# Kernel optimization log

Hardware: AMD Instinct MI355X
Metric: run time of the kernel (lower is better)

Reference implementation:

```python
import jax, jax.numpy as jnp
import numpy as np

B, H, S, D = 16, 12, 1024, 64  # batch, heads, seq, head_dim (dim=768, num_head=12)


def setup_inputs() -> dict:
    key = jax.random.key(0)
    ks = jax.random.split(key, 9)
    sc = 1.0 / np.sqrt(D)
    return {
        "x": jax.random.normal(ks[0], (B, H, S, D), dtype=jnp.float32),
        "Wq": jax.random.normal(ks[1], (D, D), dtype=jnp.float32) * sc,
        "bq": jax.random.normal(ks[2], (D,), dtype=jnp.float32) * 0.02,
        "Wk": jax.random.normal(ks[3], (D, D), dtype=jnp.float32) * sc,
        "bk": jax.random.normal(ks[4], (D,), dtype=jnp.float32) * 0.02,
        "Wv": jax.random.normal(ks[5], (D, D), dtype=jnp.float32) * sc,
        "bv": jax.random.normal(ks[6], (D,), dtype=jnp.float32) * 0.02,
        "Wo": jax.random.normal(ks[7], (D, D), dtype=jnp.float32) * sc,
        "bo": jax.random.normal(ks[8], (D,), dtype=jnp.float32) * 0.02,
    }


def reference(x, Wq, bq, Wk, bk, Wv, bv, Wo, bo):
    # torch Linear: y = x @ W^T + b, applied to last dim (head_dim)
    q = jnp.einsum("bhsd,ed->bhse", x, Wq) + bq
    k = jnp.einsum("bhsd,ed->bhse", x, Wk) + bk
    v = jnp.einsum("bhsd,ed->bhse", x, Wv) + bv
    scores = jnp.einsum("bhqd,bhkd->bhqk", q, k) / jnp.sqrt(jnp.float32(q.shape[-1]))
    attn = jax.nn.softmax(scores, axis=-1)
    out = jnp.einsum("bhqk,bhkd->bhqd", attn, v)
    out = jnp.einsum("bhsd,ed->bhse", out, Wo) + bo
    return out
```

## Files before the change

### kernel.cpp

```cpp
#include <hip/hip_runtime.h>
#include <math.h>


typedef __bf16 bf16x8 __attribute__((ext_vector_type(8)));
typedef float  f32x4  __attribute__((ext_vector_type(4)));

#define MFMA(a, b, c) __builtin_amdgcn_mfma_f32_16x16x32_bf16((a), (b), (c), 0, 0, 0)

static constexpr int S = 1024;
static constexpr int PAD = 72;
static constexpr size_t NE = 196608ull * 64ull;
static constexpr float QSCALE = 0.125f * 1.4426950408889634f;

__device__ inline unsigned long long pack4bf(float a, float b, float c, float d) {
    union { __bf16 h[4]; unsigned long long u; } pk;
    pk.h[0] = (__bf16)a; pk.h[1] = (__bf16)b; pk.h[2] = (__bf16)c; pk.h[3] = (__bf16)d;
    return pk.u;
}

__global__ void wo_conv(const float* __restrict__ Wo, __bf16* __restrict__ wob) {
    int i = (blockIdx.x * 256 + threadIdx.x) * 4;
    float4 v = *(const float4*)(Wo + i);
    *(unsigned long long*)(wob + i) = pack4bf(v.x, v.y, v.z, v.w);
}

__global__ __launch_bounds__(256) void proj_qkv(
    const float* __restrict__ x,
    const float* __restrict__ Wq, const float* __restrict__ bq,
    const float* __restrict__ Wk, const float* __restrict__ bk,
    const float* __restrict__ Wv, const float* __restrict__ bv,
    __bf16* __restrict__ gq, __bf16* __restrict__ gk, __bf16* __restrict__ gvt)
{
    __shared__ __align__(16) __bf16 lx[128][PAD];
    __shared__ __align__(16) __bf16 lw[3][64][PAD];
    __shared__ __align__(16) __bf16 lbuf[128][PAD];
    __shared__ float lb[3][64];

    const int tid = threadIdx.x;
    const int row_base = blockIdx.x * 128;

    #pragma unroll
    for (int i = tid * 4; i < 8192; i += 1024) {
        float4 v = *(const float4*)(x + (size_t)row_base * 64 + i);
        int r = i >> 6, c = i & 63;
        *(unsigned long long*)&lx[r][c] = pack4bf(v.x, v.y, v.z, v.w);
    }
    const float* Ws[3] = {Wq, Wk, Wv};
    #pragma unroll
    for (int mtx = 0; mtx < 3; mtx++) {
        #pragma unroll
        for (int i = tid * 4; i < 4096; i += 1024) {
            float4 v = *(const float4*)(Ws[mtx] + i);
            int r = i >> 6, c = i & 63;
            *(unsigned long long*)&lw[mtx][r][c] = pack4bf(v.x, v.y, v.z, v.w);
        }
    }
    if (tid < 64) { lb[0][tid] = bq[tid]; lb[1][tid] = bk[tid]; lb[2][tid] = bv[tid]; }
    __syncthreads();

    const int w = tid >> 6, lane = tid & 63, m = lane & 15, quad = lane >> 4;
    const int bh = row_base >> 10;
    const int s_base = row_base & 1023;

    bf16x8 xf[2][2];
    #pragma unroll
    for (int g = 0; g < 2; g++) {
        xf[g][0] = *(const bf16x8*)&lx[w * 32 + g * 16 + m][quad * 8];
        xf[g][1] = *(const bf16x8*)&lx[w * 32 + g * 16 + m][32 + quad * 8];
    }

    #pragma unroll
    for (int mtx = 0; mtx < 2; mtx++) {
        #pragma unroll
        for (int et = 0; et < 4; et++) {
            bf16x8 wf0 = *(const bf16x8*)&lw[mtx][et * 16 + m][quad * 8];
            bf16x8 wf1 = *(const bf16x8*)&lw[mtx][et * 16 + m][32 + quad * 8];
            float4 bias = *(const float4*)&lb[mtx][et * 16 + quad * 4];
            #pragma unroll
            for (int g = 0; g < 2; g++) {
                f32x4 acc = {0.f, 0.f, 0.f, 0.f};
                acc = MFMA(wf0, xf[g][0], acc);
                acc = MFMA(wf1, xf[g][1], acc);
                unsigned long long u;
                if (mtx == 0)
                    u = pack4bf((acc[0] + bias.x) * QSCALE, (acc[1] + bias.y) * QSCALE,
                                (acc[2] + bias.z) * QSCALE, (acc[3] + bias.w) * QSCALE);
                else
                    u = pack4bf(acc[0] + bias.x, acc[1] + bias.y,
                                acc[2] + bias.z, acc[3] + bias.w);
                *(unsigned long long*)&lbuf[w * 32 + g * 16 + m][et * 16 + quad * 4] = u;
            }
        }
        __syncthreads();
        __bf16* dst = (mtx == 0 ? gq : gk);
        #pragma unroll
        for (int it = 0; it < 4; it++) {
            int idx = it * 256 + tid;
            int row = idx >> 3, col = (idx & 7) * 8;
            *(uint4*)(dst + ((size_t)row_base + row) * 64 + col) = *(uint4*)&lbuf[row][col];
        }
        __syncthreads();
    }

    __bf16 (*lvt)[136] = (__bf16(*)[136])&lbuf[0][0];
    #pragma unroll
    for (int et = 0; et < 4; et++) {
        bf16x8 wf0 = *(const bf16x8*)&lw[2][et * 16 + m][quad * 8];
        bf16x8 wf1 = *(const bf16x8*)&lw[2][et * 16 + m][32 + quad * 8];
        const float bias = lb[2][et * 16 + m];
        #pragma unroll
        for (int g = 0; g < 2; g++) {
            f32x4 acc = {0.f, 0.f, 0.f, 0.f};
            acc = MFMA(xf[g][0], wf0, acc);
            acc = MFMA(xf[g][1], wf1, acc);
            *(unsigned long long*)&lvt[et * 16 + m][w * 32 + g * 16 + quad * 4] =
                pack4bf(acc[0] + bias, acc[1] + bias, acc[2] + bias, acc[3] + bias);
        }
    }
    __syncthreads();
    #pragma unroll
    for (int it = 0; it < 4; it++) {
        int idx = it * 256 + tid;
        int row = idx >> 4, col = (idx & 15) * 8;
        *(uint4*)(gvt + ((size_t)bh * 64 + row) * 1024 + s_base + col) = *(uint4*)&lvt[row][col];
    }
}

__global__ __launch_bounds__(256) void attn(
    const __bf16* __restrict__ gq, const __bf16* __restrict__ gk,
    const __bf16* __restrict__ gvt, const __bf16* __restrict__ wob,
    const float* __restrict__ bo, float* __restrict__ out)
{
    __shared__ __align__(16) __bf16 lk[64][PAD];
    __shared__ __align__(16) __bf16 lv[64][PAD];
    __shared__ __align__(16) __bf16 lp[4][32][PAD];

    const int tid = threadIdx.x;
    const int w = tid >> 6, lane = tid & 63, m = lane & 15, quad = lane >> 4;
    const int bh = blockIdx.x;
    const int q0 = blockIdx.y * 256 + w * 64;

    bf16x8 qf[4][2];
    #pragma unroll
    for (int g = 0; g < 4; g++) {
        const __bf16* qrow = gq + ((size_t)bh * S + q0 + g * 16 + m) * 64;
        qf[g][0] = *(const bf16x8*)(qrow + quad * 8);
        qf[g][1] = *(const bf16x8*)(qrow + 32 + quad * 8);
    }

    f32x4 o[4][4];
    float lsum[4] = {0.f, 0.f, 0.f, 0.f};
    #pragma unroll
    for (int g = 0; g < 4; g++)
        #pragma unroll
        for (int n = 0; n < 4; n++) o[g][n] = {0.f, 0.f, 0.f, 0.f};

    const int sr = tid >> 3;
    const int sc = (tid & 7) * 8;
    const __bf16* kbase = gk + (size_t)bh * S * 64;
    const __bf16* vbase = gvt + (size_t)bh * 64 * 1024;

    uint4 kreg0 = *(const uint4*)(kbase + (size_t)sr * 64 + sc);
    uint4 kreg1 = *(const uint4*)(kbase + (size_t)(sr + 32) * 64 + sc);
    uint4 vreg0 = *(const uint4*)(vbase + (size_t)sr * 1024 + sc);
    uint4 vreg1 = *(const uint4*)(vbase + (size_t)(sr + 32) * 1024 + sc);

    for (int kb = 0; kb < 16; kb++) {
        __syncthreads();
        *(uint4*)&lk[sr][sc]      = kreg0;
        *(uint4*)&lk[sr + 32][sc] = kreg1;
        *(uint4*)&lv[sr][sc]      = vreg0;
        *(uint4*)&lv[sr + 32][sc] = vreg1;
        if (kb < 15) {
            const int nb = (kb + 1) * 64;
            kreg0 = *(const uint4*)(kbase + (size_t)(nb + sr) * 64 + sc);
            kreg1 = *(const uint4*)(kbase + (size_t)(nb + sr + 32) * 64 + sc);
            vreg0 = *(const uint4*)(vbase + (size_t)sr * 1024 + nb + sc);
            vreg1 = *(const uint4*)(vbase + (size_t)(sr + 32) * 1024 + nb + sc);
        }
        __syncthreads();

        #pragma unroll
        for (int gp = 0; gp < 2; gp++) {
            #pragma unroll
            for (int t = 0; t < 4; t++) {
                bf16x8 ka0 = *(const bf16x8*)&lk[t * 16 + m][quad * 8];
                bf16x8 ka1 = *(const bf16x8*)&lk[t * 16 + m][32 + quad * 8];
                #pragma unroll
                for (int gl = 0; gl < 2; gl++) {
                    const int g = gp * 2 + gl;
                    f32x4 acc = {0.f, 0.f, 0.f, 0.f};
                    acc = MFMA(ka0, qf[g][0], acc);
                    acc = MFMA(ka1, qf[g][1], acc);
                    float e0 = __builtin_amdgcn_exp2f(acc[0]);
                    float e1 = __builtin_amdgcn_exp2f(acc[1]);
                    float e2 = __builtin_amdgcn_exp2f(acc[2]);
                    float e3 = __builtin_amdgcn_exp2f(acc[3]);
                    lsum[g] += (e0 + e1) + (e2 + e3);
                    *(unsigned long long*)&lp[w][gl * 16 + m][t * 16 + quad * 4] =
                        pack4bf(e0, e1, e2, e3);
                }
            }
            bf16x8 pb[2][2];
            #pragma unroll
            for (int gl = 0; gl < 2; gl++) {
                pb[gl][0] = *(const bf16x8*)&lp[w][gl * 16 + m][quad * 8];
                pb[gl][1] = *(const bf16x8*)&lp[w][gl * 16 + m][32 + quad * 8];
            }
            #pragma unroll
            for (int n = 0; n < 4; n++) {
                bf16x8 va0 = *(const bf16x8*)&lv[n * 16 + m][quad * 8];
                bf16x8 va1 = *(const bf16x8*)&lv[n * 16 + m][32 + quad * 8];
                #pragma unroll
                for (int gl = 0; gl < 2; gl++) {
                    const int g = gp * 2 + gl;
                    o[g][n] = MFMA(va0, pb[gl][0], o[g][n]);
                    o[g][n] = MFMA(va1, pb[gl][1], o[g][n]);
                }
            }
        }
    }

    bf16x8 wf[4][2];
    #pragma unroll
    for (int et = 0; et < 4; et++) {
        wf[et][0] = *(const bf16x8*)(wob + (size_t)(et * 16 + m) * 64 + quad * 8);
        wf[et][1] = *(const bf16x8*)(wob + (size_t)(et * 16 + m) * 64 + 32 + quad * 8);
    }
    float biasr[4];
    #pragma unroll
    for (int et = 0; et < 4; et++) biasr[et] = bo[et * 16 + m];

    #pragma unroll
    for (int g = 0; g < 4; g++) {
        lsum[g] += __shfl_xor(lsum[g], 16);
        lsum[g] += __shfl_xor(lsum[g], 32);
    }

    #pragma unroll
    for (int gp = 0; gp < 2; gp++) {
        #pragma unroll
        for (int gl = 0; gl < 2; gl++) {
            const int g = gp * 2 + gl;
            const float inv = 1.f / lsum[g];
            #pragma unroll
            for (int n = 0; n < 4; n++) {
                *(unsigned long long*)&lp[w][gl * 16 + m][n * 16 + quad * 4] =
                    pack4bf(o[g][n][0] * inv, o[g][n][1] * inv,
                            o[g][n][2] * inv, o[g][n][3] * inv);
            }
        }
        #pragma unroll
        for (int gl = 0; gl < 2; gl++) {
            const int g = gp * 2 + gl;
            bf16x8 af0 = *(const bf16x8*)&lp[w][gl * 16 + m][quad * 8];
            bf16x8 af1 = *(const bf16x8*)&lp[w][gl * 16 + m][32 + quad * 8];
            #pragma unroll
            for (int et = 0; et < 4; et++) {
                f32x4 acc = {0.f, 0.f, 0.f, 0.f};
                acc = MFMA(af0, wf[et][0], acc);
                acc = MFMA(af1, wf[et][1], acc);
                #pragma unroll
                for (int r = 0; r < 4; r++) {
                    size_t row = (size_t)bh * S + q0 + g * 16 + quad * 4 + r;
                    out[row * 64 + et * 16 + m] = acc[r] + biasr[et];
                }
            }
        }
    }
}

extern "C" void kernel_launch(void* const* d_in, const int* in_sizes, int n_in,
                              void* d_out, int out_size, void* d_ws, size_t ws_size,
                              hipStream_t stream) {
    const float* x  = (const float*)d_in[0];
    const float* Wq = (const float*)d_in[1];
    const float* bq = (const float*)d_in[2];
    const float* Wk = (const float*)d_in[3];
    const float* bk = (const float*)d_in[4];
    const float* Wv = (const float*)d_in[5];
    const float* bv = (const float*)d_in[6];
    const float* Wo = (const float*)d_in[7];
    const float* bo = (const float*)d_in[8];
    float* out = (float*)d_out;

    __bf16* gq  = (__bf16*)d_ws;
    __bf16* gk  = gq + NE;
    __bf16* gvt = gk + NE;
    __bf16* wob = gvt + NE;

    wo_conv<<<4, 256, 0, stream>>>(Wo, wob);
    proj_qkv<<<1536, 256, 0, stream>>>(x, Wq, bq, Wk, bk, Wv, bv, gq, gk, gvt);
    attn<<<dim3(192, 4), 256, 0, stream>>>(gq, gk, gvt, wob, bo, out);
}
```

Measured before the change: 213.7 us.

## Keep P and O fragments in registers by permuting V and Wo layouts

Removes the LDS round trip for the softmax probabilities and the normalized output. The exp values and the scaled O accumulators are packed directly into the bf16 MFMA operand fragments. To make this valid, the stored V-transpose positions and the Wo bf16 conversion are permuted so the MFMA reduction-dimension ordering matches the register fragment layout. This saves LDS writes, reads and space, which may raise occupancy, at the cost of a more intricate index mapping that must stay consistent across kernels.

```diff
diff --git a/kernel.cpp b/kernel.cpp
--- a/kernel.cpp
+++ b/kernel.cpp
@@ -18,10 +18,15 @@
     return pk.u;
 }
 
+union frag_u { bf16x8 v; unsigned long long u[2]; };
+
 __global__ void wo_conv(const float* __restrict__ Wo, __bf16* __restrict__ wob) {
-    int i = (blockIdx.x * 256 + threadIdx.x) * 4;
-    float4 v = *(const float4*)(Wo + i);
-    *(unsigned long long*)(wob + i) = pack4bf(v.x, v.y, v.z, v.w);
+    int p = (blockIdx.x * 256 + threadIdx.x) * 4;
+    int e = p >> 6, s = p & 63;
+    int h = s >> 5, qp = (s >> 3) & 3, tb = (s >> 2) & 1;
+    int d0 = 32 * h + 16 * tb + 4 * qp;
+    float4 v = *(const float4*)(Wo + e * 64 + d0);
+    *(unsigned long long*)(wob + p) = pack4bf(v.x, v.y, v.z, v.w);
 }
 
 __global__ __launch_bounds__(256) void proj_qkv(
@@ -113,7 +118,9 @@
             f32x4 acc = {0.f, 0.f, 0.f, 0.f};
             acc = MFMA(xf[g][0], wf0, acc);
             acc = MFMA(xf[g][1], wf1, acc);
-            *(unsigned long long*)&lvt[et * 16 + m][w * 32 + g * 16 + quad * 4] =
+            const int tp = (2 * w + g) & 3;
+            const int p0 = 64 * (w >> 1) + 32 * (tp >> 1) + 8 * quad + 4 * (tp & 1);
+            *(unsigned long long*)&lvt[et * 16 + m][p0] =
                 pack4bf(acc[0] + bias, acc[1] + bias, acc[2] + bias, acc[3] + bias);
         }
     }
@@ -133,7 +140,6 @@
 {
     __shared__ __align__(16) __bf16 lk[64][PAD];
     __shared__ __align__(16) __bf16 lv[64][PAD];
-    __shared__ __align__(16) __bf16 lp[4][32][PAD];
 
     const int tid = threadIdx.x;
     const int w = tid >> 6, lane = tid & 63, m = lane & 15, quad = lane >> 4;
@@ -182,6 +188,7 @@
 
         #pragma unroll
         for (int gp = 0; gp < 2; gp++) {
+            frag_u pb[2][2];
             #pragma unroll
             for (int t = 0; t < 4; t++) {
                 bf16x8 ka0 = *(const bf16x8*)&lk[t * 16 + m][quad * 8];
@@ -197,15 +204,8 @@
                     float e2 = __builtin_amdgcn_exp2f(acc[2]);
                     float e3 = __builtin_amdgcn_exp2f(acc[3]);
                     lsum[g] += (e0 + e1) + (e2 + e3);
-                    *(unsigned long long*)&lp[w][gl * 16 + m][t * 16 + quad * 4] =
-                        pack4bf(e0, e1, e2, e3);
+                    pb[gl][t >> 1].u[t & 1] = pack4bf(e0, e1, e2, e3);
                 }
-            }
-            bf16x8 pb[2][2];
-            #pragma unroll
-            for (int gl = 0; gl < 2; gl++) {
-                pb[gl][0] = *(const bf16x8*)&lp[w][gl * 16 + m][quad * 8];
-                pb[gl][1] = *(const bf16x8*)&lp[w][gl * 16 + m][32 + quad * 8];
             }
             #pragma unroll
             for (int n = 0; n < 4; n++) {
@@ -214,11 +214,17 @@
                 #pragma unroll
                 for (int gl = 0; gl < 2; gl++) {
                     const int g = gp * 2 + gl;
-                    o[g][n] = MFMA(va0, pb[gl][0], o[g][n]);
-                    o[g][n] = MFMA(va1, pb[gl][1], o[g][n]);
+                    o[g][n] = MFMA(va0, pb[gl][0].v, o[g][n]);
+                    o[g][n] = MFMA(va1, pb[gl][1].v, o[g][n]);
                 }
             }
         }
+    }
+
+    #pragma unroll
+    for (int g = 0; g < 4; g++) {
+        lsum[g] += __shfl_xor(lsum[g], 16);
+        lsum[g] += __shfl_xor(lsum[g], 32);
     }
 
     bf16x8 wf[4][2];
@@ -233,38 +239,21 @@
 
     #pragma unroll
     for (int g = 0; g < 4; g++) {
-        lsum[g] += __shfl_xor(lsum[g], 16);
-        lsum[g] += __shfl_xor(lsum[g], 32);
-    }
-
-    #pragma unroll
-    for (int gp = 0; gp < 2; gp++) {
-        #pragma unroll
-        for (int gl = 0; gl < 2; gl++) {
-            const int g = gp * 2 + gl;
-            const float inv = 1.f / lsum[g];
-            #pragma unroll
-            for (int n = 0; n < 4; n++) {
-                *(unsigned long long*)&lp[w][gl * 16 + m][n * 16 + quad * 4] =
-                    pack4bf(o[g][n][0] * inv, o[g][n][1] * inv,
-                            o[g][n][2] * inv, o[g][n][3] * inv);
-            }
-        }
-        #pragma unroll
-        for (int gl = 0; gl < 2; gl++) {
-            const int g = gp * 2 + gl;
-            bf16x8 af0 = *(const bf16x8*)&lp[w][gl * 16 + m][quad * 8];
-            bf16x8 af1 = *(const bf16x8*)&lp[w][gl * 16 + m][32 + quad * 8];
-            #pragma unroll
-            for (int et = 0; et < 4; et++) {
-                f32x4 acc = {0.f, 0.f, 0.f, 0.f};
-                acc = MFMA(af0, wf[et][0], acc);
-                acc = MFMA(af1, wf[et][1], acc);
-                #pragma unroll
-                for (int r = 0; r < 4; r++) {
-                    size_t row = (size_t)bh * S + q0 + g * 16 + quad * 4 + r;
-                    out[row * 64 + et * 16 + m] = acc[r] + biasr[et];
-                }
+        const float inv = 1.f / lsum[g];
+        frag_u af0, af1;
+        af0.u[0] = pack4bf(o[g][0][0] * inv, o[g][0][1] * inv, o[g][0][2] * inv, o[g][0][3] * inv);
+        af0.u[1] = pack4bf(o[g][1][0] * inv, o[g][1][1] * inv, o[g][1][2] * inv, o[g][1][3] * inv);
+        af1.u[0] = pack4bf(o[g][2][0] * inv, o[g][2][1] * inv, o[g][2][2] * inv, o[g][2][3] * inv);
+        af1.u[1] = pack4bf(o[g][3][0] * inv, o[g][3][1] * inv, o[g][3][2] * inv, o[g][3][3] * inv);
+        #pragma unroll
+        for (int et = 0; et < 4; et++) {
+            f32x4 acc = {0.f, 0.f, 0.f, 0.f};
+            acc = MFMA(af0.v, wf[et][0], acc);
+            acc = MFMA(af1.v, wf[et][1], acc);
+            #pragma unroll
+            for (int r = 0; r < 4; r++) {
+                size_t row = (size_t)bh * S + q0 + g * 16 + quad * 4 + r;
+                out[row * 64 + et * 16 + m] = acc[r] + biasr[et];
             }
         }
     }
```

After: 196.0 us. 1.09x faster.
